# Kernel tuning notes

Hardware: AMD Instinct MI355X
Metric: run time of the kernel (lower is better)

## Reference

```python
import jax, jax.numpy as jnp
import numpy as np

N, C, W = 16, 512, 4096          # batch lines, channels, max width (frames)
FINAL_DIM = 512
MASK_WIDTH = 4
NUM_NEGATIVES = 10
NUM_MASKS = 256                  # ~ mask_prob * T_total / mask_width


def _build_static():
    # Deterministic ragged lengths, already descending (pack_padded_sequence order).
    seq_len = (W - 128 * np.arange(N)).astype(np.int64)       # [4096, 3968, ..., 2176]
    t = np.arange(W)[:, None]                                  # time-major outer axis
    b = np.arange(N)[None, :]
    valid = seq_len[None, :] > t                               # [W, N]
    # pack_padded_sequence layout: for each t, all batches with len>t (desc length order)
    pack_idx = ((b * W + t)[valid]).astype(np.int64)           # [T_total] indices into flat (N*W)
    T = pack_idx.shape[0]                                      # 50176
    n_blocks = T // MASK_WIDTH
    rng = np.random.default_rng(0)
    perm = rng.permutation(n_blocks)
    sel1 = np.sort(perm[:NUM_MASKS])
    sel2 = np.sort(perm[NUM_MASKS:NUM_MASKS + NUM_NEGATIVES * NUM_MASKS])
    off = np.arange(MASK_WIDTH)
    # non-overlapping contiguous mask_width blocks, ascending (boolean-mask gather order)
    masked_idx = (sel1[:, None] * MASK_WIDTH + off).ravel().astype(np.int64)   # mask == 1
    neg_idx = (sel2[:, None] * MASK_WIDTH + off).ravel().astype(np.int64)      # mask == 2
    return seq_len, pack_idx, masked_idx, neg_idx


def setup_inputs() -> dict:
    key = jax.random.key(0)
    k1, k2, k3 = jax.random.split(key, 3)
    seq_len, pack_idx, masked_idx, neg_idx = _build_static()
    inputs = jax.random.normal(k1, (N, C, 1, W), dtype=jnp.float32)
    mask_emb = jax.random.normal(k2, (MASK_WIDTH, C), dtype=jnp.float32) * 0.02
    Wq = jax.random.normal(k3, (FINAL_DIM, C), dtype=jnp.float32) * (1.0 / np.sqrt(C))
    bq = jnp.zeros((FINAL_DIM,), dtype=jnp.float32)
    return {
        'inputs': inputs,
        'seq_len': jnp.asarray(seq_len, jnp.int32),
        'pack_idx': jnp.asarray(pack_idx, jnp.int32),
        'masked_idx': jnp.asarray(masked_idx, jnp.int32),
        'neg_idx': jnp.asarray(neg_idx, jnp.int32),
        'mask_emb': mask_emb,
        'Wq': Wq,
        'bq': bq,
    }


def reference(inputs, seq_len, pack_idx, masked_idx, neg_idx, mask_emb, Wq, bq):
    Nn, Cc, H, Ww = inputs.shape                              # H == 1
    # (N, C, 1, W) -> (N, W, 1, C) -> flat (N*W, C)
    x = jnp.transpose(inputs, (0, 3, 2, 1)).reshape(Nn * Ww, Cc)
    packed = x[pack_idx]                                      # [T_total, C] packed (time-major)
    # project_q on masked (mask==1) and negative (mask==2) token groups
    unmasked = (packed[masked_idx] @ Wq.T + bq).reshape(1, NUM_MASKS, MASK_WIDTH, FINAL_DIM)
    negatives = (packed[neg_idx] @ Wq.T + bq).reshape(NUM_NEGATIVES, NUM_MASKS, MASK_WIDTH, FINAL_DIM)
    # overwrite masked positions with the repeated mask embedding table
    packed = packed.at[masked_idx].set(jnp.tile(mask_emb, (NUM_MASKS, 1)))
    # pad_packed_sequence: scatter back to padded (N, W, C), zeros elsewhere
    out = jnp.zeros((Nn * Ww, Cc), dtype=inputs.dtype).at[pack_idx].set(packed)
    out = out.reshape(Nn, Ww, Cc).transpose(0, 2, 1)[:, :, None, :]   # (N, C, 1, W)
    return out, unmasked, negatives
```

## Files before the change

kernel.cpp:

```cpp
#include <hip/hip_runtime.h>

#define NB 16
#define CC 512
#define WW 4096
#define FD 512
#define NMASK 1024
#define T_COMB 11264
#define OUT0_ELEMS (NB*CC*WW)

#define WS_LOOKUP_OFF 0
#define WS_WQ_OFF     262144
#define WS_A_OFF      786432

#define S_LDS 36

typedef __attribute__((ext_vector_type(8))) short short8;
typedef __attribute__((ext_vector_type(4))) float f32x4;

__device__ __forceinline__ unsigned short f2bf(float x) {
  unsigned int u = __builtin_bit_cast(unsigned int, x);
  u += 0x7fffu + ((u >> 16) & 1u);
  return (unsigned short)(u >> 16);
}

__device__ __forceinline__ void gload_lds16(const void* gp, void* lp) {
  __builtin_amdgcn_global_load_lds(
      (__attribute__((address_space(1))) void*)(gp),
      (__attribute__((address_space(3))) void*)(lp),
      16, 0, 0);
}

__global__ __launch_bounds__(256) void scatter_lookup_k(
    const int* __restrict__ pack_idx, const int* __restrict__ masked_idx,
    const int* __restrict__ neg_idx, int* __restrict__ lookup) {
  int g = blockIdx.x * 256 + threadIdx.x;
  int pidx = (g < NMASK) ? masked_idx[g] : neg_idx[g - NMASK];
  lookup[pack_idx[pidx]] = g;
}

__global__ __launch_bounds__(256) void fused_copy_k(
    const float* __restrict__ in, const int* __restrict__ seq_len,
    const int* __restrict__ lookup, const float* __restrict__ mask_emb,
    const float* __restrict__ Wq, float* __restrict__ out0,
    unsigned short* __restrict__ A_ws, unsigned short* __restrict__ Wq_ws) {
  if (blockIdx.x >= 2048) {
    int b2 = blockIdx.x - 2048;
    const float4* wq4 = (const float4*)Wq;
#pragma unroll
    for (int it = 0; it < 4; ++it) {
      int i4 = it * 16384 + b2 * 256 + (int)threadIdx.x;
      float4 v = wq4[i4];
      ushort4 o;
      o.x = f2bf(v.x); o.y = f2bf(v.y); o.z = f2bf(v.z); o.w = f2bf(v.w);
      ((ushort4*)Wq_ws)[i4] = o;
    }
    return;
  }
  const int tid = threadIdx.x;
  const int bx = blockIdx.x;
  const int n = bx >> 7;
  const int w0 = (bx & 127) * 32;
  const int wl4 = (tid & 7) * 4;
  const int w = w0 + wl4;
  const int c0 = tid >> 3;
  const size_t rowbase = ((size_t)n << 21) + (size_t)w;
  float4* out4 = (float4*)out0;
  const int L = seq_len[n];

  if (w0 + 32 > L) {
    float4 z = {0.f, 0.f, 0.f, 0.f};
#pragma unroll
    for (int it = 0; it < 16; ++it) {
      int c = it * 32 + c0;
      out4[(rowbase + ((size_t)c << 12)) >> 2] = z;
    }
    return;
  }

  __shared__ unsigned short tile[CC * S_LDS];
  __shared__ int g_s[32];
  if (tid < 32) g_s[tid] = lookup[n * WW + w0 + tid];

  const int4 g4 = *(const int4*)&lookup[n * WW + w];
  const int gg[4] = {g4.x, g4.y, g4.z, g4.w};
  bool lane_has_mask = ((unsigned)gg[0] < (unsigned)NMASK) |
                       ((unsigned)gg[1] < (unsigned)NMASK) |
                       ((unsigned)gg[2] < (unsigned)NMASK) |
                       ((unsigned)gg[3] < (unsigned)NMASK);
  bool has_mask = __ballot(lane_has_mask) != 0ull;

  const float4* in4 = (const float4*)in;
#pragma unroll
  for (int it = 0; it < 16; ++it) {
    int c = it * 32 + c0;
    size_t i4 = (rowbase + ((size_t)c << 12)) >> 2;
    float4 v = in4[i4];
    ushort4 bf;
    bf.x = f2bf(v.x); bf.y = f2bf(v.y); bf.z = f2bf(v.z); bf.w = f2bf(v.w);
    *(ushort4*)&tile[c * S_LDS + wl4] = bf;
    if (has_mask) {
      float o[4] = {v.x, v.y, v.z, v.w};
#pragma unroll
      for (int k = 0; k < 4; ++k)
        if ((unsigned)gg[k] < (unsigned)NMASK)
          o[k] = mask_emb[(gg[k] & 3) * CC + c];
      v.x = o[0]; v.y = o[1]; v.z = o[2]; v.w = o[3];
    }
    out4[i4] = v;
  }
  __syncthreads();

  const int lane = tid & 63;
  bool sel = (lane < 32) && (g_s[lane & 31] >= 0);
  unsigned smask = (unsigned)__ballot(sel);
  const int c2 = tid * 2;
  while (smask) {
    int wl = __builtin_ctz(smask);
    smask &= smask - 1;
    int g = g_s[wl];
    ushort2 val;
    val.x = tile[c2 * S_LDS + wl];
    val.y = tile[(c2 + 1) * S_LDS + wl];
    *(ushort2*)&A_ws[(size_t)g * CC + c2] = val;
  }
}

__global__ __launch_bounds__(256) void gemm_k(
    const unsigned short* __restrict__ A, const unsigned short* __restrict__ B,
    const float* __restrict__ bq, float* __restrict__ out) {
  __shared__ unsigned short As[64 * 32];
  __shared__ unsigned short Bs[128 * 32];
  const int tid = threadIdx.x;
  const int lane = tid & 63;
  const int quad = lane >> 4;
  const int r16 = lane & 15;
  const int wv = tid >> 6;
  const int bm = blockIdx.x * 64;
  const int bf = blockIdx.y * 128;
  const int wm = (wv & 1) * 32;
  const int wf = (wv >> 1) * 64;
  const int wbase = tid & ~63;

  f32x4 acc[2][4];
#pragma unroll
  for (int mi = 0; mi < 2; ++mi)
#pragma unroll
    for (int fi = 0; fi < 4; ++fi)
      acc[mi][fi] = (f32x4){0.f, 0.f, 0.f, 0.f};

  for (int k0 = 0; k0 < 512; k0 += 32) {
    {
      int row = tid >> 2, cg = tid & 3;
      gload_lds16(A + (size_t)(bm + row) * 512 + k0 + cg * 8, &As[wbase * 8]);
    }
#pragma unroll
    for (int it = 0; it < 2; ++it) {
      int ch = it * 256 + tid;
      int row = ch >> 2, cg = ch & 3;
      gload_lds16(B + (size_t)(bf + row) * 512 + k0 + cg * 8,
                  &Bs[(it * 256 + wbase) * 8]);
    }
    asm volatile("s_waitcnt vmcnt(0)" ::: "memory");
    __syncthreads();

    short8 a[2], b[4];
#pragma unroll
    for (int mi = 0; mi < 2; ++mi)
      a[mi] = *(const short8*)&As[(wm + mi * 16 + r16) * 32 + quad * 8];
#pragma unroll
    for (int fi = 0; fi < 4; ++fi)
      b[fi] = *(const short8*)&Bs[(wf + fi * 16 + r16) * 32 + quad * 8];
#pragma unroll
    for (int mi = 0; mi < 2; ++mi)
#pragma unroll
      for (int fi = 0; fi < 4; ++fi)
        acc[mi][fi] = __builtin_amdgcn_mfma_f32_16x16x32_bf16(
            a[mi], b[fi], acc[mi][fi], 0, 0, 0);
    __syncthreads();
  }

#pragma unroll
  for (int fi = 0; fi < 4; ++fi) {
    int f = bf + wf + fi * 16 + r16;
    float bqv = bq[f];
#pragma unroll
    for (int mi = 0; mi < 2; ++mi) {
      int m0 = bm + wm + mi * 16 + quad * 4;
#pragma unroll
      for (int r = 0; r < 4; ++r)
        out[(size_t)(m0 + r) * 512 + f] = acc[mi][fi][r] + bqv;
    }
  }
}

extern "C" void kernel_launch(void* const* d_in, const int* in_sizes, int n_in,
                              void* d_out, int out_size, void* d_ws, size_t ws_size,
                              hipStream_t stream) {
  const float* inputs    = (const float*)d_in[0];
  const int*   seq_len   = (const int*)d_in[1];
  const int*   pack_idx  = (const int*)d_in[2];
  const int*   masked_idx= (const int*)d_in[3];
  const int*   neg_idx   = (const int*)d_in[4];
  const float* mask_emb  = (const float*)d_in[5];
  const float* Wq        = (const float*)d_in[6];
  const float* bq        = (const float*)d_in[7];
  float* out = (float*)d_out;
  char* ws = (char*)d_ws;
  int* lookup = (int*)(ws + WS_LOOKUP_OFF);
  unsigned short* wqb = (unsigned short*)(ws + WS_WQ_OFF);
  unsigned short* aws = (unsigned short*)(ws + WS_A_OFF);

  hipMemsetAsync(lookup, 0xFF, NB * WW * sizeof(int), stream);
  scatter_lookup_k<<<44, 256, 0, stream>>>(pack_idx, masked_idx, neg_idx, lookup);
  fused_copy_k<<<2112, 256, 0, stream>>>(inputs, seq_len, lookup, mask_emb, Wq,
                                         out, aws, wqb);
  gemm_k<<<dim3(176, 4), 256, 0, stream>>>(aws, wqb, bq, out + OUT0_ELEMS);
}
```

Measured before the change: 298.6 us.

## Double-buffer GEMM with swizzled LDS, nontemporal copies, skip unused bf16 tile

The GEMM now uses a K-tile of 64 with double-buffered LDS staging and an XOR-swizzled layout, so the next tile's loads overlap the MFMAs and bank conflicts are reduced. The copy kernel switches to nontemporal loads and stores for the large streaming input and output. It also skips the bf16 conversion, LDS write, sync and gather when no column in the wave's block is selected. Risks are more LDS use per GEMM block, which lowers occupancy, and a possible early return before __syncthreads if has_sel is not uniform across the block.

```diff
diff --git a/kernel.cpp b/kernel.cpp
--- a/kernel.cpp
+++ b/kernel.cpp
@@ -16,6 +16,7 @@
 
 typedef __attribute__((ext_vector_type(8))) short short8;
 typedef __attribute__((ext_vector_type(4))) float f32x4;
+typedef __attribute__((ext_vector_type(4))) unsigned short u16x4;
 
 __device__ __forceinline__ unsigned short f2bf(float x) {
   unsigned int u = __builtin_bit_cast(unsigned int, x);
@@ -45,14 +46,14 @@
     unsigned short* __restrict__ A_ws, unsigned short* __restrict__ Wq_ws) {
   if (blockIdx.x >= 2048) {
     int b2 = blockIdx.x - 2048;
-    const float4* wq4 = (const float4*)Wq;
+    const f32x4* wq4 = (const f32x4*)Wq;
 #pragma unroll
     for (int it = 0; it < 4; ++it) {
       int i4 = it * 16384 + b2 * 256 + (int)threadIdx.x;
-      float4 v = wq4[i4];
-      ushort4 o;
-      o.x = f2bf(v.x); o.y = f2bf(v.y); o.z = f2bf(v.z); o.w = f2bf(v.w);
-      ((ushort4*)Wq_ws)[i4] = o;
+      f32x4 v = wq4[i4];
+      u16x4 o;
+      o[0] = f2bf(v[0]); o[1] = f2bf(v[1]); o[2] = f2bf(v[2]); o[3] = f2bf(v[3]);
+      ((u16x4*)Wq_ws)[i4] = o;
     }
     return;
   }
@@ -64,15 +65,15 @@
   const int w = w0 + wl4;
   const int c0 = tid >> 3;
   const size_t rowbase = ((size_t)n << 21) + (size_t)w;
-  float4* out4 = (float4*)out0;
+  f32x4* out4 = (f32x4*)out0;
   const int L = seq_len[n];
 
   if (w0 + 32 > L) {
-    float4 z = {0.f, 0.f, 0.f, 0.f};
+    f32x4 z = {0.f, 0.f, 0.f, 0.f};
 #pragma unroll
     for (int it = 0; it < 16; ++it) {
       int c = it * 32 + c0;
-      out4[(rowbase + ((size_t)c << 12)) >> 2] = z;
+      __builtin_nontemporal_store(z, &out4[(rowbase + ((size_t)c << 12)) >> 2]);
     }
     return;
   }
@@ -87,27 +88,33 @@
                        ((unsigned)gg[1] < (unsigned)NMASK) |
                        ((unsigned)gg[2] < (unsigned)NMASK) |
                        ((unsigned)gg[3] < (unsigned)NMASK);
+  bool lane_has_sel = (gg[0] >= 0) | (gg[1] >= 0) | (gg[2] >= 0) | (gg[3] >= 0);
   bool has_mask = __ballot(lane_has_mask) != 0ull;
-
-  const float4* in4 = (const float4*)in;
+  bool has_sel = __ballot(lane_has_sel) != 0ull;
+
+  const f32x4* in4 = (const f32x4*)in;
 #pragma unroll
   for (int it = 0; it < 16; ++it) {
     int c = it * 32 + c0;
     size_t i4 = (rowbase + ((size_t)c << 12)) >> 2;
-    float4 v = in4[i4];
-    ushort4 bf;
-    bf.x = f2bf(v.x); bf.y = f2bf(v.y); bf.z = f2bf(v.z); bf.w = f2bf(v.w);
-    *(ushort4*)&tile[c * S_LDS + wl4] = bf;
+    f32x4 v = __builtin_nontemporal_load(&in4[i4]);
+    if (has_sel) {
+      u16x4 bf;
+      bf[0] = f2bf(v[0]); bf[1] = f2bf(v[1]);
+      bf[2] = f2bf(v[2]); bf[3] = f2bf(v[3]);
+      *(u16x4*)&tile[c * S_LDS + wl4] = bf;
+    }
     if (has_mask) {
-      float o[4] = {v.x, v.y, v.z, v.w};
+      float o[4] = {v[0], v[1], v[2], v[3]};
 #pragma unroll
       for (int k = 0; k < 4; ++k)
         if ((unsigned)gg[k] < (unsigned)NMASK)
           o[k] = mask_emb[(gg[k] & 3) * CC + c];
-      v.x = o[0]; v.y = o[1]; v.z = o[2]; v.w = o[3];
-    }
-    out4[i4] = v;
-  }
+      v[0] = o[0]; v[1] = o[1]; v[2] = o[2]; v[3] = o[3];
+    }
+    __builtin_nontemporal_store(v, &out4[i4]);
+  }
+  if (!has_sel) return;
   __syncthreads();
 
   const int lane = tid & 63;
@@ -128,8 +135,8 @@
 __global__ __launch_bounds__(256) void gemm_k(
     const unsigned short* __restrict__ A, const unsigned short* __restrict__ B,
     const float* __restrict__ bq, float* __restrict__ out) {
-  __shared__ unsigned short As[64 * 32];
-  __shared__ unsigned short Bs[128 * 32];
+  __shared__ unsigned short As[2][64 * 64];
+  __shared__ unsigned short Bs[2][128 * 64];
   const int tid = threadIdx.x;
   const int lane = tid & 63;
   const int quad = lane >> 4;
@@ -148,36 +155,64 @@
     for (int fi = 0; fi < 4; ++fi)
       acc[mi][fi] = (f32x4){0.f, 0.f, 0.f, 0.f};
 
-  for (int k0 = 0; k0 < 512; k0 += 32) {
-    {
-      int row = tid >> 2, cg = tid & 3;
-      gload_lds16(A + (size_t)(bm + row) * 512 + k0 + cg * 8, &As[wbase * 8]);
-    }
-#pragma unroll
-    for (int it = 0; it < 2; ++it) {
-      int ch = it * 256 + tid;
-      int row = ch >> 2, cg = ch & 3;
-      gload_lds16(B + (size_t)(bf + row) * 512 + k0 + cg * 8,
-                  &Bs[(it * 256 + wbase) * 8]);
-    }
-    asm volatile("s_waitcnt vmcnt(0)" ::: "memory");
+#define STAGE_TILES(buf, k0)                                                  \
+  do {                                                                        \
+    _Pragma("unroll")                                                         \
+    for (int it = 0; it < 2; ++it) {                                          \
+      int ch = it * 256 + tid;                                                \
+      int row = ch >> 3;                                                      \
+      int l = (ch & 7) ^ (row & 7);                                           \
+      gload_lds16(A + (size_t)(bm + row) * 512 + (k0) + l * 8,                \
+                  &As[buf][(it * 256 + wbase) * 8]);                          \
+    }                                                                         \
+    _Pragma("unroll")                                                         \
+    for (int it = 0; it < 4; ++it) {                                          \
+      int ch = it * 256 + tid;                                                \
+      int row = ch >> 3;                                                      \
+      int l = (ch & 7) ^ (row & 7);                                           \
+      gload_lds16(B + (size_t)(bf + row) * 512 + (k0) + l * 8,                \
+                  &Bs[buf][(it * 256 + wbase) * 8]);                          \
+    }                                                                         \
+  } while (0)
+
+  STAGE_TILES(0, 0);
+  __syncthreads();
+
+#pragma unroll
+  for (int t = 0; t < 8; ++t) {
+    const int cur = t & 1;
+    if (t < 7) STAGE_TILES(cur ^ 1, (t + 1) * 64);
+
+    short8 a[2][2], b[4][2];
+#pragma unroll
+    for (int mi = 0; mi < 2; ++mi) {
+      int row = wm + mi * 16 + r16;
+      int base = row * 64;
+      int rx = (row & 7) << 3;
+#pragma unroll
+      for (int ks = 0; ks < 2; ++ks)
+        a[mi][ks] = *(const short8*)&As[cur][base + ((((ks * 4 + quad) << 3)) ^ rx)];
+    }
+#pragma unroll
+    for (int fi = 0; fi < 4; ++fi) {
+      int row = wf + fi * 16 + r16;
+      int base = row * 64;
+      int rx = (row & 7) << 3;
+#pragma unroll
+      for (int ks = 0; ks < 2; ++ks)
+        b[fi][ks] = *(const short8*)&Bs[cur][base + ((((ks * 4 + quad) << 3)) ^ rx)];
+    }
+#pragma unroll
+    for (int ks = 0; ks < 2; ++ks)
+#pragma unroll
+      for (int mi = 0; mi < 2; ++mi)
+#pragma unroll
+        for (int fi = 0; fi < 4; ++fi)
+          acc[mi][fi] = __builtin_amdgcn_mfma_f32_16x16x32_bf16(
+              a[mi][ks], b[fi][ks], acc[mi][fi], 0, 0, 0);
     __syncthreads();
-
-    short8 a[2], b[4];
-#pragma unroll
-    for (int mi = 0; mi < 2; ++mi)
-      a[mi] = *(const short8*)&As[(wm + mi * 16 + r16) * 32 + quad * 8];
-#pragma unroll
-    for (int fi = 0; fi < 4; ++fi)
-      b[fi] = *(const short8*)&Bs[(wf + fi * 16 + r16) * 32 + quad * 8];
-#pragma unroll
-    for (int mi = 0; mi < 2; ++mi)
-#pragma unroll
-      for (int fi = 0; fi < 4; ++fi)
-        acc[mi][fi] = __builtin_amdgcn_mfma_f32_16x16x32_bf16(
-            a[mi], b[fi], acc[mi][fi], 0, 0, 0);
-    __syncthreads();
-  }
+  }
+#undef STAGE_TILES
 
 #pragma unroll
   for (int fi = 0; fi < 4; ++fi) {
@@ -188,7 +223,8 @@
       int m0 = bm + wm + mi * 16 + quad * 4;
 #pragma unroll
       for (int r = 0; r < 4; ++r)
-        out[(size_t)(m0 + r) * 512 + f] = acc[mi][fi][r] + bqv;
+        __builtin_nontemporal_store(acc[mi][fi][r] + bqv,
+                                    &out[(size_t)(m0 + r) * 512 + f]);
     }
   }
 }
@@ -210,7 +246,7 @@
   unsigned short* wqb = (unsigned short*)(ws + WS_WQ_OFF);
   unsigned short* aws = (unsigned short*)(ws + WS_A_OFF);
 
-  hipMemsetAsync(lookup, 0xFF, NB * WW * sizeof(int), stream);
+  (void)hipMemsetAsync(lookup, 0xFF, NB * WW * sizeof(int), stream);
   scatter_lookup_k<<<44, 256, 0, stream>>>(pack_idx, masked_idx, neg_idx, lookup);
   fused_copy_k<<<2112, 256, 0, stream>>>(inputs, seq_len, lookup, mask_emb, Wq,
                                          out, aws, wqb);
```

Result: faster. 285.1 us (-4.5%).
